# Kernel optimization log

Measured on AMD Instinct MI355X. Metric: run time of the kernel, lower is better.

## Reference

```python
import jax, jax.numpy as jnp
import numpy as np

NEG_SLOPE = 0.2  # PyG GATConv default negative_slope


def gat_conv(x, src, dst, W, a_src, a_dst, b, concat):
    """One GATConv layer (PyG semantics, self-loops already included in src/dst).

    x: [N, F_in]; src, dst: [E] int; W: [F_in, H*C]; a_src, a_dst: [H, C]; b: bias.
    """
    N = x.shape[0]
    H, C = a_src.shape
    h = (x @ W).reshape(N, H, C)                      # projected node features
    alpha_src = jnp.sum(h * a_src, axis=-1)           # [N, H]
    alpha_dst = jnp.sum(h * a_dst, axis=-1)           # [N, H]
    logits = jax.nn.leaky_relu(alpha_src[src] + alpha_dst[dst], NEG_SLOPE)  # [E, H]
    # softmax over incoming edges of each destination node (numerically stable)
    m = jax.ops.segment_max(logits, dst, num_segments=N)                    # [N, H]
    p = jnp.exp(logits - m[dst])
    denom = jax.ops.segment_sum(p, dst, num_segments=N)                     # [N, H]
    alpha = p / denom[dst]                                                  # [E, H]
    # attention-weighted scatter-add aggregation
    out = jax.ops.segment_sum(alpha[:, :, None] * h[src], dst, num_segments=N)  # [N, H, C]
    out = out.reshape(N, H * C) if concat else out.mean(axis=1)
    return out + b


def setup_inputs() -> dict:
    key = jax.random.key(0)
    ks = jax.random.split(key, 10)
    N, E = 50000, 800000
    nfeats, hidden, nclasses, in_head, out_head = 256, 32, 40, 8, 1
    s = 0.05
    return {
        "x": jax.random.normal(ks[0], (N, nfeats), dtype=jnp.float32),
        "edge_index": jax.random.randint(ks[1], (2, E), 0, N, dtype=jnp.int32),
        "w1": jax.random.normal(ks[2], (nfeats, in_head * hidden), dtype=jnp.float32) * s,
        "a_src1": jax.random.normal(ks[3], (in_head, hidden), dtype=jnp.float32) * s,
        "a_dst1": jax.random.normal(ks[4], (in_head, hidden), dtype=jnp.float32) * s,
        "b1": jnp.zeros((in_head * hidden,), dtype=jnp.float32),
        "w2": jax.random.normal(ks[5], (in_head * hidden, out_head * nclasses), dtype=jnp.float32) * s,
        "a_src2": jax.random.normal(ks[6], (out_head, nclasses), dtype=jnp.float32) * s,
        "a_dst2": jax.random.normal(ks[7], (out_head, nclasses), dtype=jnp.float32) * s,
        "b2": jnp.zeros((nclasses,), dtype=jnp.float32),
    }


def reference(x, edge_index, w1, a_src1, a_dst1, b1, w2, a_src2, a_dst2, b2):
    N = x.shape[0]
    loops = jnp.arange(N, dtype=edge_index.dtype)
    src = jnp.concatenate([edge_index[0], loops])  # PyG add_self_loops=True
    dst = jnp.concatenate([edge_index[1], loops])
    h = gat_conv(x, src, dst, w1, a_src1, a_dst1, b1, concat=True)
    h = jax.nn.elu(h)
    out = gat_conv(h, src, dst, w2, a_src2, a_dst2, b2, concat=False)
    return out
```

## Files before the change

### kernel.cpp

```cpp
#include <hip/hip_runtime.h>
#include <cstdint>
#include <cstddef>

constexpr int Nn   = 50000;
constexpr int Ee   = 800000;
constexpr int ETot = Ee + Nn;
constexpr int H1   = 8;
constexpr int C1h  = 32;
constexpr int HC1  = 256;
constexpr int C2   = 40;
constexpr int S2   = 64;
constexpr float SLOPE = 0.2f;
constexpr int NB_SCAN = (Nn + 255) / 256;

typedef __attribute__((ext_vector_type(8))) short bf16x8;
typedef __attribute__((ext_vector_type(4))) float f32x4;

__device__ __forceinline__ ushort f2bf(float f) {
    uint u = __float_as_uint(f);
    u += 0x7fffu + ((u >> 16) & 1u);
    return (ushort)(u >> 16);
}
__device__ __forceinline__ float bf2f(ushort b) {
    return __uint_as_float(((uint)b) << 16);
}

__device__ __forceinline__ void gload16(const void* g, void* lds) {
    typedef const __attribute__((address_space(1))) unsigned int GU;
    typedef __attribute__((address_space(3))) unsigned int LU;
    __builtin_amdgcn_global_load_lds((GU*)g, (LU*)lds, 16, 0, 0);
}

__global__ void k_prep(const float* __restrict__ w1, ushort* __restrict__ WT2,
                       const float* __restrict__ w2, ushort* __restrict__ WT2b,
                       const int* __restrict__ dstA, int* __restrict__ counts) {
    int t = blockIdx.x * blockDim.x + threadIdx.x;
    if (t < ETot) {
        int d = (t < Ee) ? dstA[t] : t - Ee;
        atomicAdd(&counts[d], 1);
    }
    if (t < 256 * 256) {
        int k = t >> 8, col = t & 255;
        float w = w1[(size_t)k * 256 + col];
        ushort h = f2bf(w), l = f2bf(w - bf2f(h));
        int kb = k >> 3, kr = k & 7;
        WT2[((size_t)(kb)      * 256 + col) * 8 + kr] = h;
        WT2[((size_t)(kb + 32) * 256 + col) * 8 + kr] = l;
    }
    if (t < 256 * 48) {
        int k = t / 48, col = t % 48;
        float w = (col < C2) ? w2[(size_t)k * C2 + col] : 0.f;
        ushort h = f2bf(w), l = f2bf(w - bf2f(h));
        int kb = k >> 3, kr = k & 7;
        WT2b[((size_t)(kb)      * 48 + col) * 8 + kr] = h;
        WT2b[((size_t)(kb + 32) * 48 + col) * 8 + kr] = l;
    }
}

__global__ __launch_bounds__(256) void k_scan_block(const int* __restrict__ counts,
                                                    int* __restrict__ exsc,
                                                    int* __restrict__ bsum) {
    __shared__ int sm[256];
    int i = blockIdx.x * 256 + threadIdx.x;
    int v = (i < Nn) ? counts[i] : 0;
    sm[threadIdx.x] = v;
    __syncthreads();
#pragma unroll
    for (int off = 1; off < 256; off <<= 1) {
        int t = (threadIdx.x >= off) ? sm[threadIdx.x - off] : 0;
        __syncthreads();
        sm[threadIdx.x] += t;
        __syncthreads();
    }
    if (i < Nn) exsc[i] = sm[threadIdx.x] - v;
    if (threadIdx.x == 255) bsum[blockIdx.x] = sm[255];
}

__global__ __launch_bounds__(256) void k_finalize2(const int* __restrict__ exsc,
                                                   const int* __restrict__ bsum,
                                                   int* __restrict__ row_off,
                                                   int* __restrict__ cursor) {
    __shared__ int sm[256];
    int t = threadIdx.x;
    int v = (t < NB_SCAN) ? bsum[t] : 0;
    sm[t] = v;
    __syncthreads();
#pragma unroll
    for (int off = 1; off < 256; off <<= 1) {
        int x = (t >= off) ? sm[t - off] : 0;
        __syncthreads();
        sm[t] += x;
        __syncthreads();
    }
    int i = blockIdx.x * 256 + t;
    if (i < Nn) {
        int r = exsc[i] + sm[blockIdx.x] - bsum[blockIdx.x];
        row_off[i] = r;
        cursor[i] = r;
    }
    if (i == 0) row_off[Nn] = ETot;
}

__global__ void k_scatter(const int* __restrict__ srcA, const int* __restrict__ dstA,
                          int* __restrict__ cursor, int* __restrict__ csr_src) {
    int e = blockIdx.x * blockDim.x + threadIdx.x;
    if (e >= ETot) return;
    int s, d;
    if (e < Ee) { s = srcA[e]; d = dstA[e]; } else { s = e - Ee; d = s; }
    int pos = atomicAdd(&cursor[d], 1);
    csr_src[pos] = s;
}

__global__ __launch_bounds__(256, 3) void k_gemm1_mfma(const float* __restrict__ x,
                                                       const ushort* __restrict__ WT2,
                                                       ushort* __restrict__ h1b,
                                                       const float* __restrict__ a_s,
                                                       const float* __restrict__ a_d,
                                                       float* __restrict__ asrc1,
                                                       float* __restrict__ adst1, int M) {
    __shared__ __align__(16) ushort AsH[2][64 * 32];
    __shared__ __align__(16) ushort AsL[2][64 * 32];
    const int tid = threadIdx.x;
    const int bm = blockIdx.x * 64;
    const int lane = tid & 63;
    const int w = tid >> 6;
    const int l16 = lane & 15, lk = lane >> 4;

    const int sakc = tid >> 6, sarow = tid & 63;
    int arow = bm + sarow; arow = arow < M ? arow : M - 1;
    const float* aptr = x + (size_t)arow * 256 + sakc * 8;
    const int sidx = (sakc * 64 + sarow) * 8;

    float4 f0, f1;
    auto loadA = [&](int t) {
        f0 = *(const float4*)(aptr + t * 32);
        f1 = *(const float4*)(aptr + t * 32 + 4);
    };
    auto cvtWrite = [&](int buf) {
        float ff[8] = {f0.x, f0.y, f0.z, f0.w, f1.x, f1.y, f1.z, f1.w};
        ushort hh[8], ll[8];
#pragma unroll
        for (int j = 0; j < 8; j++) {
            hh[j] = f2bf(ff[j]);
            ll[j] = f2bf(ff[j] - bf2f(hh[j]));
        }
        *(uint4*)(AsH[buf] + sidx) = *(uint4*)hh;
        *(uint4*)(AsL[buf] + sidx) = *(uint4*)ll;
    };

    f32x4 acc[4][4] = {};
    loadA(0);
    cvtWrite(0);
    __syncthreads();
    for (int t = 0; t < 8; t++) {
        int buf = t & 1;
        if (t + 1 < 8) loadA(t + 1);
        bf16x8 aH[4], aL[4];
#pragma unroll
        for (int m = 0; m < 4; m++) {
            aH[m] = *(const bf16x8*)(AsH[buf] + (lk * 64 + m * 16 + l16) * 8);
            aL[m] = *(const bf16x8*)(AsL[buf] + (lk * 64 + m * 16 + l16) * 8);
        }
        bf16x8 bH[4], bL[4];
#pragma unroll
        for (int n = 0; n < 4; n++) {
            bH[n] = *(const bf16x8*)(WT2 +
                ((size_t)(t * 4 + lk) * 256 + w * 64 + n * 16 + l16) * 8);
            bL[n] = *(const bf16x8*)(WT2 +
                ((size_t)(32 + t * 4 + lk) * 256 + w * 64 + n * 16 + l16) * 8);
        }
#pragma unroll
        for (int m = 0; m < 4; m++)
#pragma unroll
            for (int n = 0; n < 4; n++) {
                acc[m][n] = __builtin_amdgcn_mfma_f32_16x16x32_bf16(aH[m], bH[n], acc[m][n], 0, 0, 0);
                acc[m][n] = __builtin_amdgcn_mfma_f32_16x16x32_bf16(aH[m], bL[n], acc[m][n], 0, 0, 0);
                acc[m][n] = __builtin_amdgcn_mfma_f32_16x16x32_bf16(aL[m], bH[n], acc[m][n], 0, 0, 0);
            }
        if (t + 1 < 8) cvtWrite((t + 1) & 1);
        __syncthreads();
    }
    float as_v[4], ad_v[4];
#pragma unroll
    for (int n = 0; n < 4; n++) {
        int col = w * 64 + n * 16 + l16;
        as_v[n] = a_s[col];
        ad_v[n] = a_d[col];
    }
#pragma unroll
    for (int m = 0; m < 4; m++) {
#pragma unroll
        for (int j = 0; j < 4; j++) {
            int row = bm + m * 16 + lk * 4 + j;
            float ps0 = acc[m][0][j] * as_v[0] + acc[m][1][j] * as_v[1];
            float ps1 = acc[m][2][j] * as_v[2] + acc[m][3][j] * as_v[3];
            float pd0 = acc[m][0][j] * ad_v[0] + acc[m][1][j] * ad_v[1];
            float pd1 = acc[m][2][j] * ad_v[2] + acc[m][3][j] * ad_v[3];
#pragma unroll
            for (int off = 1; off < 16; off <<= 1) {
                ps0 += __shfl_xor(ps0, off);
                ps1 += __shfl_xor(ps1, off);
                pd0 += __shfl_xor(pd0, off);
                pd1 += __shfl_xor(pd1, off);
            }
            if (row < M) {
#pragma unroll
                for (int n = 0; n < 4; n++)
                    h1b[(size_t)row * 256 + w * 64 + n * 16 + l16] = f2bf(acc[m][n][j]);
                if (l16 == 0) {
                    asrc1[(size_t)row * H1 + w * 2]     = ps0;
                    asrc1[(size_t)row * H1 + w * 2 + 1] = ps1;
                    adst1[(size_t)row * H1 + w * 2]     = pd0;
                    adst1[(size_t)row * H1 + w * 2 + 1] = pd1;
                }
            }
        }
    }
}

__global__ __launch_bounds__(256, 4) void k_gemm2_mfma(const ushort* __restrict__ hi,
                                                       const ushort* __restrict__ lo,
                                                       const ushort* __restrict__ WT,
                                                       ushort* __restrict__ h2,
                                                       const float* __restrict__ a_s,
                                                       const float* __restrict__ a_d,
                                                       float* __restrict__ asrc2,
                                                       float* __restrict__ adst2, int M) {
    __shared__ __align__(16) ushort As[2][64 * 32];
    const int tid = threadIdx.x;
    const int bm = blockIdx.x * 64;
    const int lane = tid & 63;
    const int w = tid >> 6;
    const int l16 = lane & 15, lk = lane >> 4;

    const int sakc = tid >> 6, sarow = tid & 63;
    int arow = bm + sarow; arow = arow < M ? arow : M - 1;

    auto stageA = [&](int buf, int t) {
        const ushort* xsec = (t < 8) ? hi : lo;
        int ks = (t & 7) * 32;
        gload16(xsec + (size_t)arow * 256 + ks + sakc * 8, As[buf] + tid * 8);
    };

    f32x4 acc[3] = {};
    stageA(0, 0);
    __syncthreads();
    int buf = 0;
    for (int t = 0; t < 16; t++) {
        if (t + 1 < 16) stageA(buf ^ 1, t + 1);
        int kc = t & 7;
        bf16x8 a2 = *(const bf16x8*)(As[buf] + (lk * 64 + w * 16 + l16) * 8);
        bf16x8 bh[3];
#pragma unroll
        for (int n = 0; n < 3; n++)
            bh[n] = *(const bf16x8*)(WT +
                ((size_t)(kc * 4 + lk) * 48 + n * 16 + l16) * 8);
#pragma unroll
        for (int n = 0; n < 3; n++)
            acc[n] = __builtin_amdgcn_mfma_f32_16x16x32_bf16(a2, bh[n], acc[n], 0, 0, 0);
        if (t < 8) {
            bf16x8 bl[3];
#pragma unroll
            for (int n = 0; n < 3; n++)
                bl[n] = *(const bf16x8*)(WT +
                    ((size_t)(32 + kc * 4 + lk) * 48 + n * 16 + l16) * 8);
#pragma unroll
            for (int n = 0; n < 3; n++)
                acc[n] = __builtin_amdgcn_mfma_f32_16x16x32_bf16(a2, bl[n], acc[n], 0, 0, 0);
        }
        __syncthreads();
        buf ^= 1;
    }
    float asv[3], adv[3];
#pragma unroll
    for (int n = 0; n < 3; n++) {
        int col = n * 16 + l16;
        asv[n] = (col < C2) ? a_s[col] : 0.f;
        adv[n] = (col < C2) ? a_d[col] : 0.f;
    }
#pragma unroll
    for (int j = 0; j < 4; j++) {
        int row = bm + w * 16 + lk * 4 + j;
        float ps = acc[0][j] * asv[0] + acc[1][j] * asv[1] + acc[2][j] * asv[2];
        float pd = acc[0][j] * adv[0] + acc[1][j] * adv[1] + acc[2][j] * adv[2];
#pragma unroll
        for (int off = 1; off < 16; off <<= 1) {
            ps += __shfl_xor(ps, off);
            pd += __shfl_xor(pd, off);
        }
        if (row < M) {
#pragma unroll
            for (int n = 0; n < 3; n++)
                h2[(size_t)row * S2 + n * 16 + l16] = f2bf(acc[n][j]);
            if (l16 == 0) { asrc2[row] = ps; adst2[row] = pd; }
        }
    }
}

__global__ __launch_bounds__(256) void k_gat_aggr1(const int* __restrict__ row_off,
                                                   const int* __restrict__ csr_src,
                                                   const float* __restrict__ asrc,
                                                   const float* __restrict__ adst,
                                                   const ushort* __restrict__ h1b,
                                                   const float* __restrict__ bias,
                                                   ushort* __restrict__ o_hi,
                                                   ushort* __restrict__ o_lo) {
    int wid = (blockIdx.x * 256 + threadIdx.x) >> 6;
    if (wid >= Nn) return;
    int lane = threadIdx.x & 63;
    int half = lane >> 5, l32 = lane & 31;
    int head = l32 >> 2;
    int c0 = l32 * 8;
    int beg = row_off[wid], end = row_off[wid + 1];
    float ad = adst[(size_t)wid * H1 + head];
    float acc[8] = {};
    float sump = 0.f;
    int i = beg + half;
    for (; i + 6 < end; i += 8) {
        int s0 = csr_src[i],     s1 = csr_src[i + 2];
        int s2 = csr_src[i + 4], s3 = csr_src[i + 6];
        float a0 = asrc[(size_t)s0 * H1 + head], a1 = asrc[(size_t)s1 * H1 + head];
        float a2 = asrc[(size_t)s2 * H1 + head], a3 = asrc[(size_t)s3 * H1 + head];
        bf16x8 v0 = *(const bf16x8*)(h1b + (size_t)s0 * HC1 + c0);
        bf16x8 v1 = *(const bf16x8*)(h1b + (size_t)s1 * HC1 + c0);
        bf16x8 v2 = *(const bf16x8*)(h1b + (size_t)s2 * HC1 + c0);
        bf16x8 v3 = *(const bf16x8*)(h1b + (size_t)s3 * HC1 + c0);
        float l0 = a0 + ad; l0 = l0 > 0.f ? l0 : SLOPE * l0;
        float l1 = a1 + ad; l1 = l1 > 0.f ? l1 : SLOPE * l1;
        float l2 = a2 + ad; l2 = l2 > 0.f ? l2 : SLOPE * l2;
        float l3 = a3 + ad; l3 = l3 > 0.f ? l3 : SLOPE * l3;
        float p0 = __expf(l0), p1 = __expf(l1), p2 = __expf(l2), p3 = __expf(l3);
        sump += (p0 + p1) + (p2 + p3);
#pragma unroll
        for (int j = 0; j < 8; j++)
            acc[j] += (p0 * bf2f((ushort)v0[j]) + p1 * bf2f((ushort)v1[j])) +
                      (p2 * bf2f((ushort)v2[j]) + p3 * bf2f((ushort)v3[j]));
    }
    for (; i < end; i += 2) {
        int s = csr_src[i];
        float a = asrc[(size_t)s * H1 + head];
        bf16x8 v = *(const bf16x8*)(h1b + (size_t)s * HC1 + c0);
        float l = a + ad; l = l > 0.f ? l : SLOPE * l;
        float p = __expf(l);
        sump += p;
#pragma unroll
        for (int j = 0; j < 8; j++) acc[j] += p * bf2f((ushort)v[j]);
    }
    sump += __shfl_xor(sump, 32);
#pragma unroll
    for (int j = 0; j < 8; j++) acc[j] += __shfl_xor(acc[j], 32);
    if (half) return;
    float inv = 1.f / sump;
    float4 b0 = *(const float4*)(bias + c0);
    float4 b1 = *(const float4*)(bias + c0 + 4);
    float bb[8] = {b0.x, b0.y, b0.z, b0.w, b1.x, b1.y, b1.z, b1.w};
    uint4 uh, ul;
    uint* uhp = (uint*)&uh; uint* ulp = (uint*)&ul;
#pragma unroll
    for (int q = 0; q < 4; q++) {
        float r0 = acc[2 * q] * inv + bb[2 * q];
        float r1 = acc[2 * q + 1] * inv + bb[2 * q + 1];
        r0 = r0 > 0.f ? r0 : __expf(r0) - 1.f;
        r1 = r1 > 0.f ? r1 : __expf(r1) - 1.f;
        ushort h0 = f2bf(r0), h1v = f2bf(r1);
        ushort l0 = f2bf(r0 - bf2f(h0)), l1v = f2bf(r1 - bf2f(h1v));
        uhp[q] = (uint)h0 | ((uint)h1v << 16);
        ulp[q] = (uint)l0 | ((uint)l1v << 16);
    }
    *(uint4*)(o_hi + (size_t)wid * HC1 + c0) = uh;
    *(uint4*)(o_lo + (size_t)wid * HC1 + c0) = ul;
}

__global__ __launch_bounds__(256) void k_gat_aggr2(const int* __restrict__ row_off,
                                                   const int* __restrict__ csr_src,
                                                   const float* __restrict__ asrc,
                                                   const float* __restrict__ adst,
                                                   const ushort* __restrict__ h2,
                                                   const float* __restrict__ bias,
                                                   float* __restrict__ out) {
    int gw = (blockIdx.x * 256 + threadIdx.x) >> 6;
    int lane = threadIdx.x & 63;
    int half = lane >> 5, l32 = lane & 31;
    int wid = gw * 2 + half;
    if (wid >= Nn) return;
    int c = l32 * 2;
    int beg = row_off[wid], end = row_off[wid + 1];
    float ad = adst[wid];
    float acc0 = 0.f, acc1 = 0.f, sump = 0.f;
    int i = beg;
    for (; i + 3 < end; i += 4) {
        int s0 = csr_src[i], s1 = csr_src[i + 1], s2 = csr_src[i + 2], s3 = csr_src[i + 3];
        float a0 = asrc[s0], a1 = asrc[s1], a2 = asrc[s2], a3 = asrc[s3];
        uint u0 = *(const uint*)(h2 + (size_t)s0 * S2 + c);
        uint u1 = *(const uint*)(h2 + (size_t)s1 * S2 + c);
        uint u2 = *(const uint*)(h2 + (size_t)s2 * S2 + c);
        uint u3 = *(const uint*)(h2 + (size_t)s3 * S2 + c);
        float l0 = a0 + ad; l0 = l0 > 0.f ? l0 : SLOPE * l0;
        float l1 = a1 + ad; l1 = l1 > 0.f ? l1 : SLOPE * l1;
        float l2 = a2 + ad; l2 = l2 > 0.f ? l2 : SLOPE * l2;
        float l3 = a3 + ad; l3 = l3 > 0.f ? l3 : SLOPE * l3;
        float p0 = __expf(l0), p1 = __expf(l1), p2 = __expf(l2), p3 = __expf(l3);
        sump += (p0 + p1) + (p2 + p3);
        acc0 += p0 * bf2f((ushort)(u0 & 0xffff)) + p1 * bf2f((ushort)(u1 & 0xffff)) +
                p2 * bf2f((ushort)(u2 & 0xffff)) + p3 * bf2f((ushort)(u3 & 0xffff));
        acc1 += p0 * bf2f((ushort)(u0 >> 16)) + p1 * bf2f((ushort)(u1 >> 16)) +
                p2 * bf2f((ushort)(u2 >> 16)) + p3 * bf2f((ushort)(u3 >> 16));
    }
    for (; i < end; i++) {
        int s = csr_src[i];
        float l = asrc[s] + ad;
        l = l > 0.f ? l : SLOPE * l;
        float pe = __expf(l);
        sump += pe;
        uint u = *(const uint*)(h2 + (size_t)s * S2 + c);
        acc0 += pe * bf2f((ushort)(u & 0xffff));
        acc1 += pe * bf2f((ushort)(u >> 16));
    }
    if (c < C2) {
        float inv = 1.f / sump;
        float2 r;
        r.x = acc0 * inv + bias[c];
        r.y = acc1 * inv + bias[c + 1];
        *(float2*)(out + (size_t)wid * C2 + c) = r;
    }
}

extern "C" void kernel_launch(void* const* d_in, const int* in_sizes, int n_in,
                              void* d_out, int out_size, void* d_ws, size_t ws_size,
                              hipStream_t stream) {
    const float* x   = (const float*)d_in[0];
    const int*   ei  = (const int*)d_in[1];
    const float* w1  = (const float*)d_in[2];
    const float* as1 = (const float*)d_in[3];
    const float* ad1 = (const float*)d_in[4];
    const float* b1  = (const float*)d_in[5];
    const float* w2  = (const float*)d_in[6];
    const float* as2 = (const float*)d_in[7];
    const float* ad2 = (const float*)d_in[8];
    const float* b2  = (const float*)d_in[9];
    float* outp = (float*)d_out;

    const int* srcA = ei;
    const int* dstA = ei + Ee;

    char* W = (char*)d_ws;
    size_t o = 0;
    auto allocB = [&](size_t bytes) { void* p = W + o; o += (bytes + 255) & ~(size_t)255; return p; };

    ushort* o1hi  = (ushort*)allocB((size_t)Nn * HC1 * 2);
    ushort* o1lo  = (ushort*)allocB((size_t)Nn * HC1 * 2);
    ushort* wt2   = (ushort*)allocB((size_t)512 * 256 * 2);
    ushort* wt2b  = (ushort*)allocB((size_t)512 * 48 * 2);
    ushort* h1b   = (ushort*)allocB((size_t)Nn * HC1 * 2);
    ushort* h2    = (ushort*)allocB((size_t)Nn * S2 * 2);
    float*  asrc1 = (float*)allocB((size_t)Nn * H1 * 4);
    float*  adst1 = (float*)allocB((size_t)Nn * H1 * 4);
    float*  asrc2 = (float*)allocB((size_t)Nn * 4);
    float*  adst2 = (float*)allocB((size_t)Nn * 4);
    int* counts   = (int*)allocB((size_t)Nn * 4);
    int* exsc     = (int*)allocB((size_t)Nn * 4);
    int* bsum     = (int*)allocB(256 * 4);
    int* row_off  = (int*)allocB((size_t)(Nn + 1) * 4);
    int* cursor   = (int*)allocB((size_t)Nn * 4);
    int* csr_src  = (int*)allocB((size_t)ETot * 4);

    hipMemsetAsync(counts, 0, (size_t)Nn * sizeof(int), stream);
    k_prep<<<(ETot + 255) / 256, 256, 0, stream>>>(w1, wt2, w2, wt2b, dstA, counts);

    k_scan_block<<<NB_SCAN, 256, 0, stream>>>(counts, exsc, bsum);
    k_finalize2<<<NB_SCAN, 256, 0, stream>>>(exsc, bsum, row_off, cursor);
    k_scatter<<<(ETot + 255) / 256, 256, 0, stream>>>(srcA, dstA, cursor, csr_src);

    k_gemm1_mfma<<<(Nn + 63) / 64, 256, 0, stream>>>(
        x, wt2, h1b, as1, ad1, asrc1, adst1, Nn);
    k_gat_aggr1<<<(int)(((size_t)Nn * 64 + 255) / 256), 256, 0, stream>>>(
        row_off, csr_src, asrc1, adst1, h1b, b1, o1hi, o1lo);

    k_gemm2_mfma<<<(Nn + 63) / 64, 256, 0, stream>>>(
        o1hi, o1lo, wt2b, h2, as2, ad2, asrc2, adst2, Nn);
    int waves2 = (Nn + 1) / 2;
    k_gat_aggr2<<<(int)(((size_t)waves2 * 64 + 255) / 256), 256, 0, stream>>>(
        row_off, csr_src, asrc2, adst2, h2, b2, outp);
}
```

Measured before the change: 265.4 us.

## Switch split-bf16 GEMMs and intermediates to single-pass fp16

Both GEMMs used a three-term bf16 hi/lo split to emulate fp32. They now use a single fp16 MFMA per tile, with weights, activations and intermediates (h1, o1, h2) stored as fp16. This cuts MFMA work roughly threefold, drops the lo-part buffers and the extra traffic they cost in the layer-1 output and GEMM2 input, and simplifies the aggregation epilogue. The trade-off is accuracy: fp16 has fewer mantissa bits than the emulated path and limited range. The aggregation gathers were also split from one 16-byte load into two 8-byte loads.

```diff
diff --git a/kernel.cpp b/kernel.cpp
--- a/kernel.cpp
+++ b/kernel.cpp
@@ -13,16 +13,17 @@
 constexpr float SLOPE = 0.2f;
 constexpr int NB_SCAN = (Nn + 255) / 256;
 
-typedef __attribute__((ext_vector_type(8))) short bf16x8;
+typedef _Float16 f16x8 __attribute__((ext_vector_type(8)));
 typedef __attribute__((ext_vector_type(4))) float f32x4;
 
-__device__ __forceinline__ ushort f2bf(float f) {
-    uint u = __float_as_uint(f);
-    u += 0x7fffu + ((u >> 16) & 1u);
-    return (ushort)(u >> 16);
-}
-__device__ __forceinline__ float bf2f(ushort b) {
-    return __uint_as_float(((uint)b) << 16);
+__device__ __forceinline__ ushort f2h(float f) {
+    _Float16 h = (_Float16)f;
+    ushort u; __builtin_memcpy(&u, &h, 2);
+    return u;
+}
+__device__ __forceinline__ float h2f(ushort u) {
+    _Float16 h; __builtin_memcpy(&h, &u, 2);
+    return (float)h;
 }
 
 __device__ __forceinline__ void gload16(const void* g, void* lds) {
@@ -42,18 +43,14 @@
     if (t < 256 * 256) {
         int k = t >> 8, col = t & 255;
         float w = w1[(size_t)k * 256 + col];
-        ushort h = f2bf(w), l = f2bf(w - bf2f(h));
         int kb = k >> 3, kr = k & 7;
-        WT2[((size_t)(kb)      * 256 + col) * 8 + kr] = h;
-        WT2[((size_t)(kb + 32) * 256 + col) * 8 + kr] = l;
+        WT2[((size_t)kb * 256 + col) * 8 + kr] = f2h(w);
     }
     if (t < 256 * 48) {
         int k = t / 48, col = t % 48;
         float w = (col < C2) ? w2[(size_t)k * C2 + col] : 0.f;
-        ushort h = f2bf(w), l = f2bf(w - bf2f(h));
         int kb = k >> 3, kr = k & 7;
-        WT2b[((size_t)(kb)      * 48 + col) * 8 + kr] = h;
-        WT2b[((size_t)(kb + 32) * 48 + col) * 8 + kr] = l;
+        WT2b[((size_t)kb * 48 + col) * 8 + kr] = f2h(w);
     }
 }
 
@@ -118,8 +115,7 @@
                                                        const float* __restrict__ a_d,
                                                        float* __restrict__ asrc1,
                                                        float* __restrict__ adst1, int M) {
-    __shared__ __align__(16) ushort AsH[2][64 * 32];
-    __shared__ __align__(16) ushort AsL[2][64 * 32];
+    __shared__ __align__(16) ushort As[2][64 * 32];
     const int tid = threadIdx.x;
     const int bm = blockIdx.x * 64;
     const int lane = tid & 63;
@@ -138,14 +134,10 @@
     };
     auto cvtWrite = [&](int buf) {
         float ff[8] = {f0.x, f0.y, f0.z, f0.w, f1.x, f1.y, f1.z, f1.w};
-        ushort hh[8], ll[8];
-#pragma unroll
-        for (int j = 0; j < 8; j++) {
-            hh[j] = f2bf(ff[j]);
-            ll[j] = f2bf(ff[j] - bf2f(hh[j]));
-        }
-        *(uint4*)(AsH[buf] + sidx) = *(uint4*)hh;
-        *(uint4*)(AsL[buf] + sidx) = *(uint4*)ll;
+        ushort hh[8];
+#pragma unroll
+        for (int j = 0; j < 8; j++) hh[j] = f2h(ff[j]);
+        *(uint4*)(As[buf] + sidx) = *(uint4*)hh;
     };
 
     f32x4 acc[4][4] = {};
@@ -155,28 +147,20 @@
     for (int t = 0; t < 8; t++) {
         int buf = t & 1;
         if (t + 1 < 8) loadA(t + 1);
-        bf16x8 aH[4], aL[4];
-#pragma unroll
-        for (int m = 0; m < 4; m++) {
-            aH[m] = *(const bf16x8*)(AsH[buf] + (lk * 64 + m * 16 + l16) * 8);
-            aL[m] = *(const bf16x8*)(AsL[buf] + (lk * 64 + m * 16 + l16) * 8);
-        }
-        bf16x8 bH[4], bL[4];
-#pragma unroll
-        for (int n = 0; n < 4; n++) {
-            bH[n] = *(const bf16x8*)(WT2 +
+        f16x8 a[4];
+#pragma unroll
+        for (int m = 0; m < 4; m++)
+            a[m] = *(const f16x8*)(As[buf] + (lk * 64 + m * 16 + l16) * 8);
+        f16x8 b[4];
+#pragma unroll
+        for (int n = 0; n < 4; n++)
+            b[n] = *(const f16x8*)(WT2 +
                 ((size_t)(t * 4 + lk) * 256 + w * 64 + n * 16 + l16) * 8);
-            bL[n] = *(const bf16x8*)(WT2 +
-                ((size_t)(32 + t * 4 + lk) * 256 + w * 64 + n * 16 + l16) * 8);
-        }
 #pragma unroll
         for (int m = 0; m < 4; m++)
 #pragma unroll
-            for (int n = 0; n < 4; n++) {
-                acc[m][n] = __builtin_amdgcn_mfma_f32_16x16x32_bf16(aH[m], bH[n], acc[m][n], 0, 0, 0);
-                acc[m][n] = __builtin_amdgcn_mfma_f32_16x16x32_bf16(aH[m], bL[n], acc[m][n], 0, 0, 0);
-                acc[m][n] = __builtin_amdgcn_mfma_f32_16x16x32_bf16(aL[m], bH[n], acc[m][n], 0, 0, 0);
-            }
+            for (int n = 0; n < 4; n++)
+                acc[m][n] = __builtin_amdgcn_mfma_f32_16x16x32_f16(a[m], b[n], acc[m][n], 0, 0, 0);
         if (t + 1 < 8) cvtWrite((t + 1) & 1);
         __syncthreads();
     }
@@ -206,7 +190,7 @@
             if (row < M) {
 #pragma unroll
                 for (int n = 0; n < 4; n++)
-                    h1b[(size_t)row * 256 + w * 64 + n * 16 + l16] = f2bf(acc[m][n][j]);
+                    h1b[(size_t)row * 256 + w * 64 + n * 16 + l16] = f2h(acc[m][n][j]);
                 if (l16 == 0) {
                     asrc1[(size_t)row * H1 + w * 2]     = ps0;
                     asrc1[(size_t)row * H1 + w * 2 + 1] = ps1;
@@ -218,8 +202,7 @@
     }
 }
 
-__global__ __launch_bounds__(256, 4) void k_gemm2_mfma(const ushort* __restrict__ hi,
-                                                       const ushort* __restrict__ lo,
+__global__ __launch_bounds__(256, 4) void k_gemm2_mfma(const ushort* __restrict__ o1,
                                                        const ushort* __restrict__ WT,
                                                        ushort* __restrict__ h2,
                                                        const float* __restrict__ a_s,
@@ -237,37 +220,24 @@
     int arow = bm + sarow; arow = arow < M ? arow : M - 1;
 
     auto stageA = [&](int buf, int t) {
-        const ushort* xsec = (t < 8) ? hi : lo;
-        int ks = (t & 7) * 32;
-        gload16(xsec + (size_t)arow * 256 + ks + sakc * 8, As[buf] + tid * 8);
+        gload16(o1 + (size_t)arow * 256 + t * 32 + sakc * 8, As[buf] + tid * 8);
     };
 
     f32x4 acc[3] = {};
     stageA(0, 0);
     __syncthreads();
     int buf = 0;
-    for (int t = 0; t < 16; t++) {
-        if (t + 1 < 16) stageA(buf ^ 1, t + 1);
-        int kc = t & 7;
-        bf16x8 a2 = *(const bf16x8*)(As[buf] + (lk * 64 + w * 16 + l16) * 8);
-        bf16x8 bh[3];
+    for (int t = 0; t < 8; t++) {
+        if (t + 1 < 8) stageA(buf ^ 1, t + 1);
+        f16x8 a2 = *(const f16x8*)(As[buf] + (lk * 64 + w * 16 + l16) * 8);
+        f16x8 b2[3];
 #pragma unroll
         for (int n = 0; n < 3; n++)
-            bh[n] = *(const bf16x8*)(WT +
-                ((size_t)(kc * 4 + lk) * 48 + n * 16 + l16) * 8);
+            b2[n] = *(const f16x8*)(WT +
+                ((size_t)(t * 4 + lk) * 48 + n * 16 + l16) * 8);
 #pragma unroll
         for (int n = 0; n < 3; n++)
-            acc[n] = __builtin_amdgcn_mfma_f32_16x16x32_bf16(a2, bh[n], acc[n], 0, 0, 0);
-        if (t < 8) {
-            bf16x8 bl[3];
-#pragma unroll
-            for (int n = 0; n < 3; n++)
-                bl[n] = *(const bf16x8*)(WT +
-                    ((size_t)(32 + kc * 4 + lk) * 48 + n * 16 + l16) * 8);
-#pragma unroll
-            for (int n = 0; n < 3; n++)
-                acc[n] = __builtin_amdgcn_mfma_f32_16x16x32_bf16(a2, bl[n], acc[n], 0, 0, 0);
-        }
+            acc[n] = __builtin_amdgcn_mfma_f32_16x16x32_f16(a2, b2[n], acc[n], 0, 0, 0);
         __syncthreads();
         buf ^= 1;
     }
@@ -291,7 +261,7 @@
         if (row < M) {
 #pragma unroll
             for (int n = 0; n < 3; n++)
-                h2[(size_t)row * S2 + n * 16 + l16] = f2bf(acc[n][j]);
+                h2[(size_t)row * S2 + n * 16 + l16] = f2h(acc[n][j]);
             if (l16 == 0) { asrc2[row] = ps; adst2[row] = pd; }
         }
     }
@@ -303,8 +273,7 @@
                                                    const float* __restrict__ adst,
                                                    const ushort* __restrict__ h1b,
                                                    const float* __restrict__ bias,
-                                                   ushort* __restrict__ o_hi,
-                                                   ushort* __restrict__ o_lo) {
+                                                   ushort* __restrict__ o1) {
     int wid = (blockIdx.x * 256 + threadIdx.x) >> 6;
     if (wid >= Nn) return;
     int lane = threadIdx.x & 63;
@@ -321,30 +290,40 @@
         int s2 = csr_src[i + 4], s3 = csr_src[i + 6];
         float a0 = asrc[(size_t)s0 * H1 + head], a1 = asrc[(size_t)s1 * H1 + head];
         float a2 = asrc[(size_t)s2 * H1 + head], a3 = asrc[(size_t)s3 * H1 + head];
-        bf16x8 v0 = *(const bf16x8*)(h1b + (size_t)s0 * HC1 + c0);
-        bf16x8 v1 = *(const bf16x8*)(h1b + (size_t)s1 * HC1 + c0);
-        bf16x8 v2 = *(const bf16x8*)(h1b + (size_t)s2 * HC1 + c0);
-        bf16x8 v3 = *(const bf16x8*)(h1b + (size_t)s3 * HC1 + c0);
+        ushort4 w0 = *(const ushort4*)(h1b + (size_t)s0 * HC1 + c0);
+        ushort4 w0b = *(const ushort4*)(h1b + (size_t)s0 * HC1 + c0 + 4);
+        ushort4 w1 = *(const ushort4*)(h1b + (size_t)s1 * HC1 + c0);
+        ushort4 w1b = *(const ushort4*)(h1b + (size_t)s1 * HC1 + c0 + 4);
+        ushort4 w2 = *(const ushort4*)(h1b + (size_t)s2 * HC1 + c0);
+        ushort4 w2b = *(const ushort4*)(h1b + (size_t)s2 * HC1 + c0 + 4);
+        ushort4 w3 = *(const ushort4*)(h1b + (size_t)s3 * HC1 + c0);
+        ushort4 w3b = *(const ushort4*)(h1b + (size_t)s3 * HC1 + c0 + 4);
         float l0 = a0 + ad; l0 = l0 > 0.f ? l0 : SLOPE * l0;
         float l1 = a1 + ad; l1 = l1 > 0.f ? l1 : SLOPE * l1;
         float l2 = a2 + ad; l2 = l2 > 0.f ? l2 : SLOPE * l2;
         float l3 = a3 + ad; l3 = l3 > 0.f ? l3 : SLOPE * l3;
         float p0 = __expf(l0), p1 = __expf(l1), p2 = __expf(l2), p3 = __expf(l3);
         sump += (p0 + p1) + (p2 + p3);
+        ushort v0[8] = {w0.x, w0.y, w0.z, w0.w, w0b.x, w0b.y, w0b.z, w0b.w};
+        ushort v1[8] = {w1.x, w1.y, w1.z, w1.w, w1b.x, w1b.y, w1b.z, w1b.w};
+        ushort v2[8] = {w2.x, w2.y, w2.z, w2.w, w2b.x, w2b.y, w2b.z, w2b.w};
+        ushort v3[8] = {w3.x, w3.y, w3.z, w3.w, w3b.x, w3b.y, w3b.z, w3b.w};
 #pragma unroll
         for (int j = 0; j < 8; j++)
-            acc[j] += (p0 * bf2f((ushort)v0[j]) + p1 * bf2f((ushort)v1[j])) +
-                      (p2 * bf2f((ushort)v2[j]) + p3 * bf2f((ushort)v3[j]));
+            acc[j] += (p0 * h2f(v0[j]) + p1 * h2f(v1[j])) +
+                      (p2 * h2f(v2[j]) + p3 * h2f(v3[j]));
     }
     for (; i < end; i += 2) {
         int s = csr_src[i];
         float a = asrc[(size_t)s * H1 + head];
-        bf16x8 v = *(const bf16x8*)(h1b + (size_t)s * HC1 + c0);
+        ushort4 wv = *(const ushort4*)(h1b + (size_t)s * HC1 + c0);
+        ushort4 wb = *(const ushort4*)(h1b + (size_t)s * HC1 + c0 + 4);
         float l = a + ad; l = l > 0.f ? l : SLOPE * l;
         float p = __expf(l);
         sump += p;
-#pragma unroll
-        for (int j = 0; j < 8; j++) acc[j] += p * bf2f((ushort)v[j]);
+        ushort v[8] = {wv.x, wv.y, wv.z, wv.w, wb.x, wb.y, wb.z, wb.w};
+#pragma unroll
+        for (int j = 0; j < 8; j++) acc[j] += p * h2f(v[j]);
     }
     sump += __shfl_xor(sump, 32);
 #pragma unroll
@@ -354,21 +333,14 @@
     float4 b0 = *(const float4*)(bias + c0);
     float4 b1 = *(const float4*)(bias + c0 + 4);
     float bb[8] = {b0.x, b0.y, b0.z, b0.w, b1.x, b1.y, b1.z, b1.w};
-    uint4 uh, ul;
-    uint* uhp = (uint*)&uh; uint* ulp = (uint*)&ul;
-#pragma unroll
-    for (int q = 0; q < 4; q++) {
-        float r0 = acc[2 * q] * inv + bb[2 * q];
-        float r1 = acc[2 * q + 1] * inv + bb[2 * q + 1];
-        r0 = r0 > 0.f ? r0 : __expf(r0) - 1.f;
-        r1 = r1 > 0.f ? r1 : __expf(r1) - 1.f;
-        ushort h0 = f2bf(r0), h1v = f2bf(r1);
-        ushort l0 = f2bf(r0 - bf2f(h0)), l1v = f2bf(r1 - bf2f(h1v));
-        uhp[q] = (uint)h0 | ((uint)h1v << 16);
-        ulp[q] = (uint)l0 | ((uint)l1v << 16);
-    }
-    *(uint4*)(o_hi + (size_t)wid * HC1 + c0) = uh;
-    *(uint4*)(o_lo + (size_t)wid * HC1 + c0) = ul;
+    ushort hh[8];
+#pragma unroll
+    for (int j = 0; j < 8; j++) {
+        float r = acc[j] * inv + bb[j];
+        r = r > 0.f ? r : __expf(r) - 1.f;
+        hh[j] = f2h(r);
+    }
+    *(uint4*)(o1 + (size_t)wid * HC1 + c0) = *(uint4*)hh;
 }
 
 __global__ __launch_bounds__(256) void k_gat_aggr2(const int* __restrict__ row_off,
@@ -401,10 +373,10 @@
         float l3 = a3 + ad; l3 = l3 > 0.f ? l3 : SLOPE * l3;
         float p0 = __expf(l0), p1 = __expf(l1), p2 = __expf(l2), p3 = __expf(l3);
         sump += (p0 + p1) + (p2 + p3);
-        acc0 += p0 * bf2f((ushort)(u0 & 0xffff)) + p1 * bf2f((ushort)(u1 & 0xffff)) +
-                p2 * bf2f((ushort)(u2 & 0xffff)) + p3 * bf2f((ushort)(u3 & 0xffff));
-        acc1 += p0 * bf2f((ushort)(u0 >> 16)) + p1 * bf2f((ushort)(u1 >> 16)) +
-                p2 * bf2f((ushort)(u2 >> 16)) + p3 * bf2f((ushort)(u3 >> 16));
+        acc0 += p0 * h2f((ushort)(u0 & 0xffff)) + p1 * h2f((ushort)(u1 & 0xffff)) +
+                p2 * h2f((ushort)(u2 & 0xffff)) + p3 * h2f((ushort)(u3 & 0xffff));
+        acc1 += p0 * h2f((ushort)(u0 >> 16)) + p1 * h2f((ushort)(u1 >> 16)) +
+                p2 * h2f((ushort)(u2 >> 16)) + p3 * h2f((ushort)(u3 >> 16));
     }
     for (; i < end; i++) {
         int s = csr_src[i];
@@ -413,8 +385,8 @@
         float pe = __expf(l);
         sump += pe;
         uint u = *(const uint*)(h2 + (size_t)s * S2 + c);
-        acc0 += pe * bf2f((ushort)(u & 0xffff));
-        acc1 += pe * bf2f((ushort)(u >> 16));
+        acc0 += pe * h2f((ushort)(u & 0xffff));
+        acc1 += pe * h2f((ushort)(u >> 16));
     }
     if (c < C2) {
         float inv = 1.f / sump;
@@ -447,10 +419,9 @@
     size_t o = 0;
     auto allocB = [&](size_t bytes) { void* p = W + o; o += (bytes + 255) & ~(size_t)255; return p; };
 
-    ushort* o1hi  = (ushort*)allocB((size_t)Nn * HC1 * 2);
-    ushort* o1lo  = (ushort*)allocB((size_t)Nn * HC1 * 2);
-    ushort* wt2   = (ushort*)allocB((size_t)512 * 256 * 2);
-    ushort* wt2b  = (ushort*)allocB((size_t)512 * 48 * 2);
+    ushort* o1    = (ushort*)allocB((size_t)Nn * HC1 * 2);
+    ushort* wt2   = (ushort*)allocB((size_t)256 * 256 * 2);
+    ushort* wt2b  = (ushort*)allocB((size_t)256 * 48 * 2);
     ushort* h1b   = (ushort*)allocB((size_t)Nn * HC1 * 2);
     ushort* h2    = (ushort*)allocB((size_t)Nn * S2 * 2);
     float*  asrc1 = (float*)allocB((size_t)Nn * H1 * 4);
@@ -474,10 +445,10 @@
     k_gemm1_mfma<<<(Nn + 63) / 64, 256, 0, stream>>>(
         x, wt2, h1b, as1, ad1, asrc1, adst1, Nn);
     k_gat_aggr1<<<(int)(((size_t)Nn * 64 + 255) / 256), 256, 0, stream>>>(
-        row_off, csr_src, asrc1, adst1, h1b, b1, o1hi, o1lo);
+        row_off, csr_src, asrc1, adst1, h1b, b1, o1);
 
     k_gemm2_mfma<<<(Nn + 63) / 64, 256, 0, stream>>>(
-        o1hi, o1lo, wt2b, h2, as2, ad2, asrc2, adst2, Nn);
+        o1, wt2b, h2, as2, ad2, asrc2, adst2, Nn);
     int waves2 = (Nn + 1) / 2;
     k_gat_aggr2<<<(int)(((size_t)waves2 * 64 + 255) / 256), 256, 0, stream>>>(
         row_off, csr_src, asrc2, adst2, h2, b2, outp);
```

After: 236.3 us, median of 2. -10.9%, faster.
